# Kernel optimization log

Measured on AMD Instinct MI355X. Metric: run time of the kernel, lower is better.

## Reference

```python
import jax, jax.numpy as jnp
import numpy as np

V, H, L, B, S = 32000, 1024, 2, 8, 256


def setup_inputs() -> dict:
    key = jax.random.key(0)
    ks = jax.random.split(key, 12)
    s = 1.0 / np.sqrt(H)  # PyTorch LSTM/Linear init range
    u = lambda k, shape: jax.random.uniform(k, shape, jnp.float32, -s, s)
    return {
        "x": jax.random.randint(ks[0], (B, S), 0, V, dtype=jnp.int32),
        "h0": jnp.zeros((L, B, H), jnp.float32),
        "c0": jnp.zeros((L, B, H), jnp.float32),
        "w_ih0": u(ks[1], (4 * H, V)),
        "w_hh0": u(ks[2], (4 * H, H)),
        "b_ih0": u(ks[3], (4 * H,)),
        "b_hh0": u(ks[4], (4 * H,)),
        "w_ih1": u(ks[5], (4 * H, H)),
        "w_hh1": u(ks[6], (4 * H, H)),
        "b_ih1": u(ks[7], (4 * H,)),
        "b_hh1": u(ks[8], (4 * H,)),
        "fc_w": u(ks[9], (V, H)),
        "fc_b": u(ks[10], (V,)),
    }


def _lstm_layer(xproj, h0, c0, w_hh):
    """xproj: [S,B,4H] input-to-gate projection (biases folded in).
    Gate order i,f,g,o matches PyTorch."""
    def step(carry, xp):
        h, c = carry
        g = xp + h @ w_hh.T  # [B,4H]
        i, f, gg, o = jnp.split(g, 4, axis=-1)
        c = jax.nn.sigmoid(f) * c + jax.nn.sigmoid(i) * jnp.tanh(gg)
        h = jax.nn.sigmoid(o) * jnp.tanh(c)
        return (h, c), h
    (hT, cT), hs = jax.lax.scan(step, (h0, c0), xproj)
    return hs, hT, cT


def reference(x, h0, c0, w_ih0, w_hh0, b_ih0, b_hh0, w_ih1, w_hh1, b_ih1, b_hh1, fc_w, fc_b):
    # F.one_hot(x, V).float() @ w_ih0.T  ==  gather of rows of w_ih0.T (identical math)
    xp0 = jnp.take(w_ih0.T, x, axis=0) + (b_ih0 + b_hh0)  # [B,S,4H]
    xp0 = xp0.transpose(1, 0, 2)  # [S,B,4H] for time-major scan
    h1s, h1T, c1T = _lstm_layer(xp0, h0[0], c0[0], w_hh0)
    xp1 = h1s @ w_ih1.T + (b_ih1 + b_hh1)  # [S,B,4H]
    h2s, h2T, c2T = _lstm_layer(xp1, h0[1], c0[1], w_hh1)
    out = h2s.transpose(1, 0, 2).reshape(-1, H)  # [B*S,H]
    logits = out @ fc_w.T + fc_b  # [B*S,V]
    hn = jnp.stack([h1T, h2T])
    cn = jnp.stack([c1T, c2T])
    return logits, (hn, cn)
```

## Files before the change

kernel.cpp:

```cpp
#include <hip/hip_runtime.h>
#include <cmath>

typedef float  f32x4  __attribute__((ext_vector_type(4)));
typedef __bf16 bf16x8 __attribute__((ext_vector_type(8)));

static constexpr int HN  = 1024;
static constexpr int VN  = 32000;
static constexpr int BN  = 8;
static constexpr int SN  = 256;
static constexpr int H4N = 4096;

__global__ __launch_bounds__(256) void k_gather(const int* __restrict__ x,
    const float* __restrict__ w_ih0, const float* __restrict__ b_ih0,
    const float* __restrict__ b_hh0, float* __restrict__ xp) {
  int bid = blockIdx.x;
  int t = bid >> 3, b = bid & 7;
  int tok = x[b * SN + t];
  const float* col = w_ih0 + tok;
  float* dst = xp + (size_t)bid * H4N;
  for (int r = threadIdx.x; r < H4N; r += 256)
    dst[r] = col[(size_t)r * VN] + b_ih0[r] + b_hh0[r];
}

__global__ __launch_bounds__(256) void k_step(const float* __restrict__ xp_t,
    const float* __restrict__ w_hh, const float* __restrict__ h_in,
    float* __restrict__ h_out, const float* __restrict__ c_in,
    float* __restrict__ c_out, float* __restrict__ hs_out,
    float* __restrict__ hn_out, float* __restrict__ cn_out, int is_last) {
  __shared__ float h_lds[BN][HN + 4];
  __shared__ float red[8][4][4][8];
  __shared__ float gates[4][4][8];
  int tid = threadIdx.x;

  #pragma unroll
  for (int j = 0; j < 8; ++j) {
    int f4 = j * 256 + tid;
    f32x4 v = *(const f32x4*)&h_in[f4 * 4];
    *(f32x4*)&h_lds[j][(f4 & 255) * 4] = v;
  }
  __syncthreads();

  int ks = tid >> 5, u = (tid >> 3) & 3, b = tid & 7;
  int unit = blockIdx.x * 4 + u;
  const float* w0 = w_hh + (size_t)unit * HN;
  const float* w1 = w0 + (size_t)HN * HN;
  const float* w2 = w1 + (size_t)HN * HN;
  const float* w3 = w2 + (size_t)HN * HN;
  int k0 = ks * 128;
  float a0 = 0.f, a1 = 0.f, a2 = 0.f, a3 = 0.f;
  #pragma unroll 8
  for (int i = 0; i < 32; ++i) {
    int k = k0 + i * 4;
    f32x4 hv = *(const f32x4*)&h_lds[b][k];
    f32x4 wv;
    wv = *(const f32x4*)&w0[k]; a0 += hv[0]*wv[0]+hv[1]*wv[1]+hv[2]*wv[2]+hv[3]*wv[3];
    wv = *(const f32x4*)&w1[k]; a1 += hv[0]*wv[0]+hv[1]*wv[1]+hv[2]*wv[2]+hv[3]*wv[3];
    wv = *(const f32x4*)&w2[k]; a2 += hv[0]*wv[0]+hv[1]*wv[1]+hv[2]*wv[2]+hv[3]*wv[3];
    wv = *(const f32x4*)&w3[k]; a3 += hv[0]*wv[0]+hv[1]*wv[1]+hv[2]*wv[2]+hv[3]*wv[3];
  }
  red[ks][u][0][b] = a0;
  red[ks][u][1][b] = a1;
  red[ks][u][2][b] = a2;
  red[ks][u][3][b] = a3;
  __syncthreads();

  if (tid < 128) {
    int rid = tid >> 3, bb = tid & 7;
    int uu = rid >> 2, g = rid & 3;
    float s = 0.f;
    #pragma unroll
    for (int q = 0; q < 8; ++q) s += red[q][uu][g][bb];
    gates[uu][g][bb] = s + xp_t[bb * H4N + g * HN + blockIdx.x * 4 + uu];
  }
  __syncthreads();

  if (tid < 32) {
    int uu = tid >> 3, bb = tid & 7;
    int un = blockIdx.x * 4 + uu;
    float gi = gates[uu][0][bb], gf = gates[uu][1][bb];
    float gg = gates[uu][2][bb], go = gates[uu][3][bb];
    float c_old = c_in[bb * HN + un];
    float si = 1.f / (1.f + expf(-gi));
    float sf = 1.f / (1.f + expf(-gf));
    float so = 1.f / (1.f + expf(-go));
    float c = sf * c_old + si * tanhf(gg);
    float h = so * tanhf(c);
    c_out[bb * HN + un] = c;
    h_out[bb * HN + un] = h;
    hs_out[bb * HN + un] = h;
    if (is_last) { hn_out[bb * HN + un] = h; cn_out[bb * HN + un] = c; }
  }
}

__global__ __launch_bounds__(256) void k_split(const float* __restrict__ src,
    __bf16* __restrict__ hi, __bf16* __restrict__ lo) {
  int i = (blockIdx.x * 256 + threadIdx.x) * 4;
  f32x4 v = *(const f32x4*)&src[i];
  #pragma unroll
  for (int j = 0; j < 4; ++j) {
    __bf16 h = (__bf16)v[j];
    hi[i + j] = h;
    lo[i + j] = (__bf16)(v[j] - (float)h);
  }
}

__global__ __launch_bounds__(256) void k_gemm(const __bf16* __restrict__ Ahi,
    const __bf16* __restrict__ Alo, const float* __restrict__ Bsrc,
    const float* __restrict__ bias1, const float* __restrict__ bias2,
    float* __restrict__ C, int Mt, int N, int permute) {
  __shared__ __bf16 sAh[128][32], sAl[128][32], sBh[128][32], sBl[128][32];
  int bid = blockIdx.x;
  int tn = bid / Mt, tm = bid % Mt;
  int tid = threadIdx.x, lane = tid & 63, wid = tid >> 6;
  int wr = wid >> 1, wc = wid & 1;
  f32x4 acc[4][4] = {};
  const size_t K = 1024;

  for (int kk = 0; kk < 1024; kk += 32) {
    __syncthreads();
    #pragma unroll
    for (int it = 0; it < 2; ++it) {
      int c = it * 256 + tid;
      int r = c >> 2, k8 = (c & 3) * 8;
      size_t ga = (size_t)(tm * 128 + r) * K + kk + k8;
      *(bf16x8*)&sAh[r][k8] = *(const bf16x8*)&Ahi[ga];
      *(bf16x8*)&sAl[r][k8] = *(const bf16x8*)&Alo[ga];
      size_t gb = (size_t)(tn * 128 + r) * K + kk + k8;
      f32x4 x0 = *(const f32x4*)&Bsrc[gb];
      f32x4 x1 = *(const f32x4*)&Bsrc[gb + 4];
      bf16x8 bh, bl;
      #pragma unroll
      for (int j = 0; j < 4; ++j) {
        __bf16 h0 = (__bf16)x0[j]; bh[j]     = h0; bl[j]     = (__bf16)(x0[j] - (float)h0);
        __bf16 h1 = (__bf16)x1[j]; bh[4 + j] = h1; bl[4 + j] = (__bf16)(x1[j] - (float)h1);
      }
      *(bf16x8*)&sBh[r][k8] = bh;
      *(bf16x8*)&sBl[r][k8] = bl;
    }
    __syncthreads();

    int kq = (lane >> 4) * 8;
    bf16x8 ah[4], al[4], bh[4], bl[4];
    #pragma unroll
    for (int i = 0; i < 4; ++i) {
      int ra = wr * 64 + i * 16 + (lane & 15);
      ah[i] = *(const bf16x8*)&sAh[ra][kq];
      al[i] = *(const bf16x8*)&sAl[ra][kq];
      int rb = wc * 64 + i * 16 + (lane & 15);
      bh[i] = *(const bf16x8*)&sBh[rb][kq];
      bl[i] = *(const bf16x8*)&sBl[rb][kq];
    }
    #pragma unroll
    for (int i = 0; i < 4; ++i)
      #pragma unroll
      for (int j = 0; j < 4; ++j) {
        acc[i][j] = __builtin_amdgcn_mfma_f32_16x16x32_bf16(ah[i], bh[j], acc[i][j], 0, 0, 0);
        acc[i][j] = __builtin_amdgcn_mfma_f32_16x16x32_bf16(ah[i], bl[j], acc[i][j], 0, 0, 0);
        acc[i][j] = __builtin_amdgcn_mfma_f32_16x16x32_bf16(al[i], bh[j], acc[i][j], 0, 0, 0);
      }
  }

  #pragma unroll
  for (int j = 0; j < 4; ++j) {
    int gcol = tn * 128 + wc * 64 + j * 16 + (lane & 15);
    float bv = bias1[gcol] + (bias2 ? bias2[gcol] : 0.f);
    #pragma unroll
    for (int i = 0; i < 4; ++i) {
      #pragma unroll
      for (int r = 0; r < 4; ++r) {
        int row = tm * 128 + wr * 64 + i * 16 + ((lane >> 4) << 2) + r;
        int orow = permute ? ((row & 7) * 256 + (row >> 3)) : row;
        C[(size_t)orow * N + gcol] = acc[i][j][r] + bv;
      }
    }
  }
}

extern "C" void kernel_launch(void* const* d_in, const int* in_sizes, int n_in,
                              void* d_out, int out_size, void* d_ws, size_t ws_size,
                              hipStream_t stream) {
  (void)in_sizes; (void)n_in; (void)out_size; (void)ws_size;
  const int*   x     = (const int*)  d_in[0];
  const float* h0    = (const float*)d_in[1];
  const float* c0    = (const float*)d_in[2];
  const float* w_ih0 = (const float*)d_in[3];
  const float* w_hh0 = (const float*)d_in[4];
  const float* b_ih0 = (const float*)d_in[5];
  const float* b_hh0 = (const float*)d_in[6];
  const float* w_ih1 = (const float*)d_in[7];
  const float* w_hh1 = (const float*)d_in[8];
  const float* b_ih1 = (const float*)d_in[9];
  const float* b_hh1 = (const float*)d_in[10];
  const float* fc_w  = (const float*)d_in[11];
  const float* fc_b  = (const float*)d_in[12];
  float* out = (float*)d_out;
  float* ws  = (float*)d_ws;

  float* xp   = ws;
  float* h1s  = ws + 8388608;
  float* h2s  = ws + 10485760;
  float* hbA  = ws + 12582912;
  float* hbB  = ws + 12591104;
  float* cbuf = ws + 12599296;
  __bf16* Ahi = (__bf16*)(ws + 12607488);
  __bf16* Alo = (__bf16*)(ws + 13656064);

  const size_t LOG = (size_t)2048 * VN;
  float* hn = out + LOG;
  float* cn = out + LOG + 16384;

  k_gather<<<SN * BN, 256, 0, stream>>>(x, w_ih0, b_ih0, b_hh0, xp);

  for (int t = 0; t < SN; ++t) {
    const float* hin = (t == 0) ? h0 : ((t & 1) ? hbB : hbA);
    float* hout = (t & 1) ? hbA : hbB;
    const float* cin = (t == 0) ? c0 : cbuf;
    k_step<<<256, 256, 0, stream>>>(xp + (size_t)t * BN * H4N, w_hh0, hin, hout,
                                    cin, cbuf, h1s + (size_t)t * BN * HN,
                                    hn, cn, t == SN - 1);
  }

  k_split<<<2048, 256, 0, stream>>>(h1s, Ahi, Alo);
  k_gemm<<<16 * 32, 256, 0, stream>>>(Ahi, Alo, w_ih1, b_ih1, b_hh1, xp,
                                      16, H4N, 0);

  for (int t = 0; t < SN; ++t) {
    const float* hin = (t == 0) ? (h0 + BN * HN) : ((t & 1) ? hbB : hbA);
    float* hout = (t & 1) ? hbA : hbB;
    const float* cin = (t == 0) ? (c0 + BN * HN) : cbuf;
    k_step<<<256, 256, 0, stream>>>(xp + (size_t)t * BN * H4N, w_hh1, hin, hout,
                                    cin, cbuf, h2s + (size_t)t * BN * HN,
                                    hn + BN * HN, cn + BN * HN, t == SN - 1);
  }

  k_split<<<2048, 256, 0, stream>>>(h2s, Ahi, Alo);
  k_gemm<<<16 * 250, 256, 0, stream>>>(Ahi, Alo, fc_w, fc_b, nullptr, out,
                                       16, VN, 1);
}
```

Before: 4.788 ms.

## Replace per-timestep LSTM launches with persistent kernel using grid barrier and LDS-resident weights

Replaces 256 per-step kernel launches per layer with one persistent kernel of 256 workgroups that loops over timesteps and synchronises through an atomic-counter grid barrier. Each workgroup loads its 16 rows of w_hh into LDS once, with an XOR swizzle, so the recurrent weights are no longer re-read from global memory every step. The cell state is kept in LDS and the matvec is re-tiled into 4x4 register blocks. The approach depends on all 256 workgroups being co-resident, otherwise the barrier deadlocks, and it adds spin-wait cost at every step.

```diff
diff --git a/kernel.cpp b/kernel.cpp
--- a/kernel.cpp
+++ b/kernel.cpp
@@ -22,73 +22,118 @@
     dst[r] = col[(size_t)r * VN] + b_ih0[r] + b_hh0[r];
 }
 
-__global__ __launch_bounds__(256) void k_step(const float* __restrict__ xp_t,
-    const float* __restrict__ w_hh, const float* __restrict__ h_in,
-    float* __restrict__ h_out, const float* __restrict__ c_in,
-    float* __restrict__ c_out, float* __restrict__ hs_out,
-    float* __restrict__ hn_out, float* __restrict__ cn_out, int is_last) {
-  __shared__ float h_lds[BN][HN + 4];
-  __shared__ float red[8][4][4][8];
-  __shared__ float gates[4][4][8];
-  int tid = threadIdx.x;
-
-  #pragma unroll
-  for (int j = 0; j < 8; ++j) {
-    int f4 = j * 256 + tid;
-    f32x4 v = *(const f32x4*)&h_in[f4 * 4];
-    *(f32x4*)&h_lds[j][(f4 & 255) * 4] = v;
-  }
+__device__ __forceinline__ void grid_sync(unsigned* bar, unsigned target) {
   __syncthreads();
-
-  int ks = tid >> 5, u = (tid >> 3) & 3, b = tid & 7;
-  int unit = blockIdx.x * 4 + u;
-  const float* w0 = w_hh + (size_t)unit * HN;
-  const float* w1 = w0 + (size_t)HN * HN;
-  const float* w2 = w1 + (size_t)HN * HN;
-  const float* w3 = w2 + (size_t)HN * HN;
-  int k0 = ks * 128;
-  float a0 = 0.f, a1 = 0.f, a2 = 0.f, a3 = 0.f;
-  #pragma unroll 8
-  for (int i = 0; i < 32; ++i) {
-    int k = k0 + i * 4;
-    f32x4 hv = *(const f32x4*)&h_lds[b][k];
-    f32x4 wv;
-    wv = *(const f32x4*)&w0[k]; a0 += hv[0]*wv[0]+hv[1]*wv[1]+hv[2]*wv[2]+hv[3]*wv[3];
-    wv = *(const f32x4*)&w1[k]; a1 += hv[0]*wv[0]+hv[1]*wv[1]+hv[2]*wv[2]+hv[3]*wv[3];
-    wv = *(const f32x4*)&w2[k]; a2 += hv[0]*wv[0]+hv[1]*wv[1]+hv[2]*wv[2]+hv[3]*wv[3];
-    wv = *(const f32x4*)&w3[k]; a3 += hv[0]*wv[0]+hv[1]*wv[1]+hv[2]*wv[2]+hv[3]*wv[3];
-  }
-  red[ks][u][0][b] = a0;
-  red[ks][u][1][b] = a1;
-  red[ks][u][2][b] = a2;
-  red[ks][u][3][b] = a3;
+  if (threadIdx.x == 0) {
+    __threadfence();
+    atomicAdd(bar, 1u);
+    while (__hip_atomic_load(bar, __ATOMIC_ACQUIRE, __HIP_MEMORY_SCOPE_AGENT) < target)
+      __builtin_amdgcn_s_sleep(1);
+  }
   __syncthreads();
-
-  if (tid < 128) {
-    int rid = tid >> 3, bb = tid & 7;
-    int uu = rid >> 2, g = rid & 3;
-    float s = 0.f;
-    #pragma unroll
-    for (int q = 0; q < 8; ++q) s += red[q][uu][g][bb];
-    gates[uu][g][bb] = s + xp_t[bb * H4N + g * HN + blockIdx.x * 4 + uu];
-  }
-  __syncthreads();
-
-  if (tid < 32) {
-    int uu = tid >> 3, bb = tid & 7;
-    int un = blockIdx.x * 4 + uu;
-    float gi = gates[uu][0][bb], gf = gates[uu][1][bb];
-    float gg = gates[uu][2][bb], go = gates[uu][3][bb];
-    float c_old = c_in[bb * HN + un];
-    float si = 1.f / (1.f + expf(-gi));
-    float sf = 1.f / (1.f + expf(-gf));
-    float so = 1.f / (1.f + expf(-go));
-    float c = sf * c_old + si * tanhf(gg);
-    float h = so * tanhf(c);
-    c_out[bb * HN + un] = c;
-    h_out[bb * HN + un] = h;
-    hs_out[bb * HN + un] = h;
-    if (is_last) { hn_out[bb * HN + un] = h; cn_out[bb * HN + un] = c; }
+}
+
+__global__ __launch_bounds__(256, 1) void k_lstm(
+    const float* __restrict__ xp,
+    const float* __restrict__ w_hh,
+    const float* __restrict__ h0,
+    const float* __restrict__ c0,
+    float* __restrict__ hs,
+    float* __restrict__ hn, float* __restrict__ cn,
+    unsigned* __restrict__ bar) {
+  __shared__ float wL[16][1024];
+  __shared__ float hL[8192];
+  __shared__ float red[8][4][4][32];
+  __shared__ float gates[16][8];
+  __shared__ float cL[32];
+
+  const int tid = threadIdx.x;
+  const int wg  = blockIdx.x;
+  const int u0  = wg * 4;
+
+  for (int it = 0; it < 16; ++it) {
+    int g = it >> 2, u = it & 3;
+    int k4 = tid;
+    int k4s = k4 ^ ((k4 >> 3) & 7);
+    f32x4 v = *(const f32x4*)&w_hh[((size_t)g * HN + u0 + u) * HN + k4 * 4];
+    *(f32x4*)&wL[it][k4s * 4] = v;
+  }
+  if (tid < 32) cL[tid] = c0[(tid & 7) * HN + u0 + (tid >> 3)];
+
+  const int ks = tid & 31, rg = (tid >> 5) & 3, bg = tid >> 7;
+  const int ksx = ks & 7;
+
+  for (int t = 0; t < SN; ++t) {
+    const float* hsrc = (t == 0) ? h0 : (hs + (size_t)(t - 1) * (BN * HN));
+    #pragma unroll
+    for (int it = 0; it < 8; ++it) {
+      int b = tid & 7, k4 = (tid >> 3) + it * 32;
+      f32x4 v = *(const f32x4*)&hsrc[b * HN + k4 * 4];
+      int idx = (k4 * 8 + b) ^ ((k4 >> 3) & 7);
+      *(f32x4*)&hL[idx * 4] = v;
+    }
+    __syncthreads();
+
+    float acc[4][4] = {};
+    #pragma unroll
+    for (int j = 0; j < 8; ++j) {
+      int k4 = ks * 8 + j;
+      int k4s = k4 ^ ksx;
+      f32x4 wv[4], hv[4];
+      #pragma unroll
+      for (int ri = 0; ri < 4; ++ri)
+        wv[ri] = *(const f32x4*)&wL[rg * 4 + ri][k4s * 4];
+      #pragma unroll
+      for (int bi = 0; bi < 4; ++bi) {
+        int idx = ((k4 << 3) | (bg * 4 + bi)) ^ ksx;
+        hv[bi] = *(const f32x4*)&hL[idx * 4];
+      }
+      #pragma unroll
+      for (int ri = 0; ri < 4; ++ri)
+        #pragma unroll
+        for (int bi = 0; bi < 4; ++bi)
+          acc[ri][bi] += wv[ri][0]*hv[bi][0] + wv[ri][1]*hv[bi][1]
+                       + wv[ri][2]*hv[bi][2] + wv[ri][3]*hv[bi][3];
+    }
+    #pragma unroll
+    for (int ri = 0; ri < 4; ++ri)
+      #pragma unroll
+      for (int bi = 0; bi < 4; ++bi)
+        red[rg * 2 + bg][ri][bi][ks] = acc[ri][bi];
+    __syncthreads();
+
+    if (tid < 128) {
+      int row = tid >> 3, b = tid & 7;
+      int rrg = row >> 2, ri = row & 3, bbg = b >> 2, bi = b & 3;
+      const float* rp = red[rrg * 2 + bbg][ri][bi];
+      float s = 0.f;
+      #pragma unroll
+      for (int q = 0; q < 32; ++q) s += rp[(q + tid) & 31];
+      int g = row >> 2, u = row & 3;
+      s += xp[(size_t)t * (BN * H4N) + b * H4N + g * HN + u0 + u];
+      gates[row][b] = s;
+    }
+    __syncthreads();
+
+    if (tid < 32) {
+      int u = tid >> 3, b = tid & 7;
+      float gi = gates[0 * 4 + u][b], gf = gates[1 * 4 + u][b];
+      float gg = gates[2 * 4 + u][b], go = gates[3 * 4 + u][b];
+      float si = 1.f / (1.f + expf(-gi));
+      float sf = 1.f / (1.f + expf(-gf));
+      float so = 1.f / (1.f + expf(-go));
+      float c = sf * cL[tid] + si * tanhf(gg);
+      float h = so * tanhf(c);
+      cL[tid] = c;
+      hs[(size_t)t * (BN * HN) + b * HN + u0 + u] = h;
+      if (t == SN - 1) {
+        hn[b * HN + u0 + u] = h;
+        cn[b * HN + u0 + u] = c;
+      }
+    }
+
+    if (t != SN - 1) grid_sync(bar, 256u * (unsigned)(t + 1));
+    else __syncthreads();
   }
 }
 
@@ -199,39 +244,26 @@
   float* xp   = ws;
   float* h1s  = ws + 8388608;
   float* h2s  = ws + 10485760;
-  float* hbA  = ws + 12582912;
-  float* hbB  = ws + 12591104;
-  float* cbuf = ws + 12599296;
-  __bf16* Ahi = (__bf16*)(ws + 12607488);
-  __bf16* Alo = (__bf16*)(ws + 13656064);
+  __bf16* Ahi = (__bf16*)(ws + 12582912);
+  __bf16* Alo = (__bf16*)(ws + 13631488);
+  unsigned* bar = (unsigned*)(ws + 14680064);
 
   const size_t LOG = (size_t)2048 * VN;
   float* hn = out + LOG;
   float* cn = out + LOG + 16384;
 
+  hipMemsetAsync(bar, 0, 2 * sizeof(unsigned), stream);
+
   k_gather<<<SN * BN, 256, 0, stream>>>(x, w_ih0, b_ih0, b_hh0, xp);
 
-  for (int t = 0; t < SN; ++t) {
-    const float* hin = (t == 0) ? h0 : ((t & 1) ? hbB : hbA);
-    float* hout = (t & 1) ? hbA : hbB;
-    const float* cin = (t == 0) ? c0 : cbuf;
-    k_step<<<256, 256, 0, stream>>>(xp + (size_t)t * BN * H4N, w_hh0, hin, hout,
-                                    cin, cbuf, h1s + (size_t)t * BN * HN,
-                                    hn, cn, t == SN - 1);
-  }
+  k_lstm<<<256, 256, 0, stream>>>(xp, w_hh0, h0, c0, h1s, hn, cn, bar + 0);
 
   k_split<<<2048, 256, 0, stream>>>(h1s, Ahi, Alo);
   k_gemm<<<16 * 32, 256, 0, stream>>>(Ahi, Alo, w_ih1, b_ih1, b_hh1, xp,
                                       16, H4N, 0);
 
-  for (int t = 0; t < SN; ++t) {
-    const float* hin = (t == 0) ? (h0 + BN * HN) : ((t & 1) ? hbB : hbA);
-    float* hout = (t & 1) ? hbA : hbB;
-    const float* cin = (t == 0) ? (c0 + BN * HN) : cbuf;
-    k_step<<<256, 256, 0, stream>>>(xp + (size_t)t * BN * H4N, w_hh1, hin, hout,
-                                    cin, cbuf, h2s + (size_t)t * BN * HN,
-                                    hn + BN * HN, cn + BN * HN, t == SN - 1);
-  }
+  k_lstm<<<256, 256, 0, stream>>>(xp, w_hh1, h0 + BN * HN, c0 + BN * HN,
+                                  h2s, hn + BN * HN, cn + BN * HN, bar + 1);
 
   k_split<<<2048, 256, 0, stream>>>(h2s, Ahi, Alo);
   k_gemm<<<16 * 250, 256, 0, stream>>>(Ahi, Alo, fc_w, fc_b, nullptr, out,
```

Result: slower. 9.229 ms (+92.8%).
